# Kernel optimization log

Hardware: AMD Instinct MI355X
Metric: run time of the kernel (lower is better)

Reference implementation:

```python
import jax, jax.numpy as jnp
import numpy as np

B, S, HID = 1, 2048, 2048
H, KH, D = 16, 8, 128          # query heads, kv heads, head_dim
GROUPS = H // KH                # num_key_value_groups = 2
EPS = 1e-6
SCALE = D ** -0.5
NEG = -1e9


def rmsnorm(x, w):
    # torch.nn.RMSNorm over last dim with learned weight
    return x * jax.lax.rsqrt(jnp.mean(x * x, axis=-1, keepdims=True) + EPS) * w


def rope(x, cos, sin):
    # x: [b, s, h, d]; cos/sin: [s, d//2]  (rotate-half style, matching apply_rotary_emb_single)
    half = x.shape[-1] // 2
    xr, xi = x[..., :half], x[..., half:]
    c = cos[None, :, None, :]
    s = sin[None, :, None, :]
    return jnp.concatenate([xr * c - xi * s, xr * s + xi * c], axis=-1)


def setup_inputs() -> dict:
    key = jax.random.key(0)
    ks = jax.random.split(key, 8)
    hidden_states = jax.random.normal(ks[0], (B, S, HID), jnp.float32)
    # real RoPE angle tables (theta=1e6, Qwen3-style), shape [S, D//2]
    inv_freq = 1.0 / (1e6 ** (np.arange(0, D, 2, dtype=np.float32) / D))
    ang = np.arange(S, dtype=np.float32)[:, None] * inv_freq[None, :]
    freqs_cos = jnp.asarray(np.cos(ang), jnp.float32)
    freqs_sin = jnp.asarray(np.sin(ang), jnp.float32)
    # additive causal mask [1, S, S]
    causal = jnp.tril(jnp.ones((S, S), jnp.bool_))
    atten_mask = jnp.where(causal, 0.0, NEG).astype(jnp.float32)[None]
    # learned params (no bias: attention_bias=False)
    Wq = jax.random.normal(ks[1], (H * D, HID), jnp.float32) * 0.02
    Wk = jax.random.normal(ks[2], (KH * D, HID), jnp.float32) * 0.02
    Wv = jax.random.normal(ks[3], (KH * D, HID), jnp.float32) * 0.02
    Wo = jax.random.normal(ks[4], (HID, H * D), jnp.float32) * 0.02
    q_norm_w = 1.0 + 0.01 * jax.random.normal(ks[5], (D,), jnp.float32)
    k_norm_w = 1.0 + 0.01 * jax.random.normal(ks[6], (D,), jnp.float32)
    return {"hidden_states": hidden_states, "freqs_cos": freqs_cos, "freqs_sin": freqs_sin,
            "atten_mask": atten_mask, "Wq": Wq, "Wk": Wk, "Wv": Wv, "Wo": Wo,
            "q_norm_w": q_norm_w, "k_norm_w": k_norm_w}


def reference(hidden_states, freqs_cos, freqs_sin, atten_mask, Wq, Wk, Wv, Wo, q_norm_w, k_norm_w):
    b, s, _ = hidden_states.shape
    q = (hidden_states @ Wq.T).reshape(b, s, H, D)
    k = (hidden_states @ Wk.T).reshape(b, s, KH, D)
    v = (hidden_states @ Wv.T).reshape(b, s, KH, D)
    q = rope(rmsnorm(q, q_norm_w), freqs_cos, freqs_sin)
    k = rope(rmsnorm(k, k_norm_w), freqs_cos, freqs_sin)
    # GQA: head i uses kv head i // GROUPS -> repeat kv heads in-order
    k_exp = jnp.repeat(k, GROUPS, axis=2)  # [b, s, H, d]
    v_exp = jnp.repeat(v, GROUPS, axis=2)
    scores = jnp.einsum('bshd,bthd->bhst', q, k_exp) * SCALE + atten_mask[:, None, :, :]
    attn = jax.nn.softmax(scores, axis=-1)
    y = jnp.einsum('bhst,bthd->bshd', attn, v_exp).reshape(b, s, H * D)
    y = y @ Wo.T
    # output_new_cache_only: last-position k (post-norm/RoPE) and raw v per kv head
    k_new = jnp.transpose(k[:, -1], (1, 0, 2))  # [KH, b, D]
    v_new = jnp.transpose(v[:, -1], (1, 0, 2))  # [KH, b, D]
    return y, k_new, v_new
```

## Files before the change

kernel.cpp:

```cpp
#include <hip/hip_runtime.h>
#include <hip/hip_bf16.h>
#include <math.h>

#define S_LEN 2048
#define HID 2048
#define NH 16
#define NKH 8
#define HD 128
#define QKV_N 4096
#define SCALE 0.08838834764831845f
#define EPS 1e-6f
#define LOG2E 1.4426950408889634f
#define QSCALE (SCALE * LOG2E)

typedef __hip_bfloat16 bf16;
typedef unsigned int u32;
typedef __bf16 bf16x8 __attribute__((ext_vector_type(8)));
typedef float f32x4 __attribute__((ext_vector_type(4)));

#define MFMA(a, b, c) __builtin_amdgcn_mfma_f32_16x16x32_bf16(a, b, c, 0, 0, 0)

static __device__ __forceinline__ bf16x8 ld_frag(const bf16* p) {
    return __builtin_bit_cast(bf16x8, *(const uint4*)p);
}

static __device__ __forceinline__ void gload_lds16(const void* g, void* l) {
    __builtin_amdgcn_global_load_lds(
        (const __attribute__((address_space(1))) u32*)g,
        (__attribute__((address_space(3))) u32*)l, 16, 0, 0);
}

__global__ __launch_bounds__(256) void cvt5(
    const float* __restrict__ s0, const float* __restrict__ s1,
    const float* __restrict__ s2, const float* __restrict__ s3,
    const float* __restrict__ s4,
    bf16* __restrict__ d0, bf16* __restrict__ d1, bf16* __restrict__ d2,
    bf16* __restrict__ d3, bf16* __restrict__ d4)
{
    int i = blockIdx.x * 256 + threadIdx.x;
    const float* s; bf16* d; int off;
    if (i < (1 << 20))                   { s = s0; d = d0; off = 0; }
    else if (i < (2 << 20))              { s = s1; d = d1; off = 1 << 20; }
    else if (i < (2 << 20) + (1 << 19))  { s = s2; d = d2; off = 2 << 20; }
    else if (i < (3 << 20))              { s = s3; d = d3; off = (2 << 20) + (1 << 19); }
    else                                 { s = s4; d = d4; off = 3 << 20; }
    int j = i - off;
    float4 v = ((const float4*)s)[j];
    bf16* p = d + 4 * (size_t)j;
    p[0] = __float2bfloat16(v.x);
    p[1] = __float2bfloat16(v.y);
    p[2] = __float2bfloat16(v.z);
    p[3] = __float2bfloat16(v.w);
}

__global__ __launch_bounds__(256, 2) void gemm_qkv(
    const bf16* __restrict__ A, const bf16* __restrict__ B,
    bf16* __restrict__ qkvb, bf16* __restrict__ vT,
    const float* __restrict__ fcos, const float* __restrict__ fsin,
    const float* __restrict__ qw, const float* __restrict__ kw,
    float* __restrict__ knew, float* __restrict__ vnew)
{
    __shared__ bf16 As[128 * 64];
    __shared__ bf16 Bs[128 * 64];
    const int tid = threadIdx.x;
    const int n0 = blockIdx.x * 128, m0 = blockIdx.y * 128;
    const int w = tid >> 6, lane = tid & 63;
    const int l15 = lane & 15, quad = lane >> 4;

    f32x4 acc[2][8];
    #pragma unroll
    for (int i = 0; i < 2; ++i)
        #pragma unroll
        for (int j = 0; j < 8; ++j)
            acc[i][j] = f32x4{0.f, 0.f, 0.f, 0.f};

    const int srow8 = lane >> 3;
    const int sls = ((lane & 7) ^ srow8) * 8;

    for (int k0 = 0; k0 < HID; k0 += 64) {
        __syncthreads();
        #pragma unroll
        for (int j = 0; j < 8; ++j) {
            int c = 8 * w + j;
            if (c < 16) {
                int row = c * 8 + srow8;
                gload_lds16(A + (size_t)(m0 + row) * HID + k0 + sls, &As[c * 512]);
            } else {
                int row = (c - 16) * 8 + srow8;
                gload_lds16(B + (size_t)(n0 + row) * HID + k0 + sls, &Bs[(c - 16) * 512]);
            }
        }
        __syncthreads();

        #pragma unroll
        for (int kc = 0; kc < 2; ++kc) {
            const int ph = ((kc * 4 + quad) ^ (l15 & 7)) * 8;
            bf16x8 av[2], bv[8];
            av[0] = ld_frag(&As[(w * 32 + l15) * 64 + ph]);
            av[1] = ld_frag(&As[(w * 32 + 16 + l15) * 64 + ph]);
            #pragma unroll
            for (int j = 0; j < 8; ++j)
                bv[j] = ld_frag(&Bs[(j * 16 + l15) * 64 + ph]);
            #pragma unroll
            for (int i = 0; i < 2; ++i)
                #pragma unroll
                for (int j = 0; j < 8; ++j)
                    acc[i][j] = MFMA(av[i], bv[j], acc[i][j]);
        }
    }

    const int hblk = n0 >> 7;
    if (hblk < 24) {
        const float* wgt = (hblk < 16) ? qw : kw;
        float wv[8];
        #pragma unroll
        for (int j = 0; j < 8; ++j) wv[j] = wgt[j * 16 + l15];
        const size_t cb = (hblk < 16) ? (size_t)hblk * HD
                                      : (size_t)HID + (size_t)(hblk - 16) * HD;
        #pragma unroll
        for (int i = 0; i < 2; ++i)
            #pragma unroll
            for (int r = 0; r < 4; ++r) {
                int srow = m0 + w * 32 + i * 16 + quad * 4 + r;
                float ss = 0.f;
                #pragma unroll
                for (int j = 0; j < 8; ++j) ss += acc[i][j][r] * acc[i][j][r];
                ss += __shfl_xor(ss, 1);
                ss += __shfl_xor(ss, 2);
                ss += __shfl_xor(ss, 4);
                ss += __shfl_xor(ss, 8);
                float rr = rsqrtf(ss * (1.0f / 128.0f) + EPS);
                float x[8], res[8];
                #pragma unroll
                for (int j = 0; j < 8; ++j) x[j] = acc[i][j][r] * rr * wv[j];
                #pragma unroll
                for (int jj = 0; jj < 4; ++jj) {
                    float c = fcos[srow * 64 + jj * 16 + l15];
                    float s = fsin[srow * 64 + jj * 16 + l15];
                    res[jj]     = x[jj] * c - x[jj + 4] * s;
                    res[jj + 4] = x[jj] * s + x[jj + 4] * c;
                }
                if (hblk < 16) {
                    #pragma unroll
                    for (int j = 0; j < 8; ++j)
                        qkvb[(size_t)srow * QKV_N + cb + j * 16 + l15] =
                            __float2bfloat16(res[j] * QSCALE);
                } else {
                    #pragma unroll
                    for (int j = 0; j < 8; ++j)
                        qkvb[(size_t)srow * QKV_N + cb + j * 16 + l15] =
                            __float2bfloat16(res[j]);
                    if (srow == S_LEN - 1) {
                        #pragma unroll
                        for (int j = 0; j < 8; ++j)
                            knew[(hblk - 16) * HD + j * 16 + l15] = res[j];
                    }
                }
            }
    } else {
        const int kh = hblk - 24;
        #pragma unroll
        for (int i = 0; i < 2; ++i) {
            int rowbase = m0 + w * 32 + i * 16 + quad * 4;
            #pragma unroll
            for (int j = 0; j < 8; ++j) {
                int d = j * 16 + l15;
                union { uint2 u; bf16 hh[4]; } pk;
                #pragma unroll
                for (int r = 0; r < 4; ++r)
                    pk.hh[r] = __float2bfloat16(acc[i][j][r]);
                *(uint2*)&vT[(size_t)(kh * HD + d) * S_LEN + rowbase] = pk.u;
                if (rowbase == S_LEN - 4)
                    vnew[kh * HD + d] = acc[i][j][3];
            }
        }
    }
}

__global__ __launch_bounds__(256, 2) void gemm_n64(
    const bf16* __restrict__ A, const bf16* __restrict__ B,
    float* __restrict__ C, int M, int N, int K)
{
    __shared__ bf16 As[128 * 64];
    __shared__ bf16 Bs[64 * 64];
    const int tid = threadIdx.x;
    const int n0 = blockIdx.x * 64, m0 = blockIdx.y * 128;
    const int w = tid >> 6, lane = tid & 63;
    const int l15 = lane & 15, quad = lane >> 4;

    f32x4 acc[2][4];
    #pragma unroll
    for (int i = 0; i < 2; ++i)
        #pragma unroll
        for (int j = 0; j < 4; ++j)
            acc[i][j] = f32x4{0.f, 0.f, 0.f, 0.f};

    const int srow8 = lane >> 3;
    const int sls = ((lane & 7) ^ srow8) * 8;

    for (int k0 = 0; k0 < K; k0 += 64) {
        __syncthreads();
        #pragma unroll
        for (int j = 0; j < 6; ++j) {
            int c = 6 * w + j;
            if (c < 16) {
                int row = c * 8 + srow8;
                gload_lds16(A + (size_t)(m0 + row) * K + k0 + sls, &As[c * 512]);
            } else {
                int row = (c - 16) * 8 + srow8;
                gload_lds16(B + (size_t)(n0 + row) * K + k0 + sls, &Bs[(c - 16) * 512]);
            }
        }
        __syncthreads();

        #pragma unroll
        for (int kc = 0; kc < 2; ++kc) {
            const int ph = ((kc * 4 + quad) ^ (l15 & 7)) * 8;
            bf16x8 av[2], bv[4];
            av[0] = ld_frag(&As[(w * 32 + l15) * 64 + ph]);
            av[1] = ld_frag(&As[(w * 32 + 16 + l15) * 64 + ph]);
            #pragma unroll
            for (int j = 0; j < 4; ++j)
                bv[j] = ld_frag(&Bs[(j * 16 + l15) * 64 + ph]);
            #pragma unroll
            for (int i = 0; i < 2; ++i)
                #pragma unroll
                for (int j = 0; j < 4; ++j)
                    acc[i][j] = MFMA(av[i], bv[j], acc[i][j]);
        }
    }

    #pragma unroll
    for (int i = 0; i < 2; ++i)
        #pragma unroll
        for (int j = 0; j < 4; ++j)
            #pragma unroll
            for (int r = 0; r < 4; ++r)
                C[(size_t)(m0 + w * 32 + i * 16 + quad * 4 + r) * N +
                  n0 + j * 16 + l15] = acc[i][j][r];
}

__global__ __launch_bounds__(256, 2) void attn_mfma(
    const bf16* __restrict__ qkvb, const bf16* __restrict__ vT,
    bf16* __restrict__ outb)
{
    __shared__ bf16 Ks[2][64 * 128];
    __shared__ bf16 Vs[2][128 * 64];
    __shared__ bf16 Ps[4][16 * 72];

    const int x = blockIdx.x;
    const int h = blockIdx.y, kvh = h >> 1;
    int a = (x & 1) ? (31 - (x >> 1)) : (x >> 1);
    const int qb = (h < 8) ? a : 31 - a;
    const int tid = threadIdx.x, w = tid >> 6, lane = tid & 63;
    const int l15 = lane & 15, quad = lane >> 4;
    const int qw0 = qb * 64 + w * 16;

    bf16x8 qf[4];
    #pragma unroll
    for (int dk = 0; dk < 4; ++dk)
        qf[dk] = ld_frag(qkvb + (size_t)(qw0 + l15) * QKV_N +
                         h * HD + dk * 32 + quad * 8);

    f32x4 o[8];
    #pragma unroll
    for (int dt = 0; dt < 8; ++dt) o[dt] = f32x4{0.f, 0.f, 0.f, 0.f};
    float l_st = 0.f;

    auto stage = [&](int t, int nb) {
        const int kt0 = t * 64;
        if (w < 2) {
            #pragma unroll
            for (int c = 0; c < 8; ++c) {
                int chunk = w * 8 + c;
                int row = 4 * chunk + (lane >> 4);
                int ls = (lane & 15) ^ (row & 15);
                gload_lds16(qkvb + (size_t)(kt0 + row) * QKV_N + HID +
                            kvh * HD + ls * 8,
                            &Ks[nb][chunk * 512]);
            }
        } else {
            #pragma unroll
            for (int c = 0; c < 8; ++c) {
                int chunk = (w - 2) * 8 + c;
                int row = 8 * chunk + (lane >> 3);
                int ls = (lane & 7) ^ ((lane >> 3) & 7);
                gload_lds16(vT + (size_t)(kvh * HD + row) * S_LEN + kt0 + ls * 8,
                            &Vs[nb][chunk * 512]);
            }
        }
    };

    stage(0, 0);
    for (int t = 0; t <= qb; ++t) {
        const int pp = t & 1;
        const int kt0 = t * 64;
        __syncthreads();
        if (t < qb) stage(t + 1, pp ^ 1);

        f32x4 sc[4];
        #pragma unroll
        for (int mt = 0; mt < 4; ++mt) sc[mt] = f32x4{0.f, 0.f, 0.f, 0.f};
        #pragma unroll
        for (int dk = 0; dk < 4; ++dk)
            #pragma unroll
            for (int mt = 0; mt < 4; ++mt) {
                bf16x8 kf = ld_frag(&Ks[pp][(mt * 16 + l15) * 128 +
                                            (((dk * 4 + quad) ^ l15) & 15) * 8]);
                sc[mt] = MFMA(kf, qf[dk], sc[mt]);
            }

        if (kt0 + 63 > qw0) {
            #pragma unroll
            for (int mt = 0; mt < 4; ++mt)
                #pragma unroll
                for (int r = 0; r < 4; ++r) {
                    int kg = kt0 + mt * 16 + quad * 4 + r;
                    if (kg > qw0 + l15) sc[mt][r] = -1e30f;
                }
        }

        #pragma unroll
        for (int mt = 0; mt < 4; ++mt) {
            union { uint2 u; bf16 hh[4]; } pk;
            #pragma unroll
            for (int r = 0; r < 4; ++r) {
                float p = exp2f(sc[mt][r]);
                pk.hh[r] = __float2bfloat16(p);
                l_st += p;
            }
            *(uint2*)&Ps[w][l15 * 72 + mt * 16 + quad * 4] = pk.u;
        }

        #pragma unroll
        for (int kc = 0; kc < 2; ++kc) {
            bf16x8 pf = ld_frag(&Ps[w][l15 * 72 + kc * 32 + quad * 8]);
            #pragma unroll
            for (int dt = 0; dt < 8; ++dt) {
                bf16x8 vf = ld_frag(&Vs[pp][(dt * 16 + l15) * 64 +
                                            (((kc * 4 + quad) ^ (l15 & 7)) * 8)]);
                o[dt] = MFMA(vf, pf, o[dt]);
            }
        }
    }

    l_st += __shfl_xor(l_st, 16, 64);
    l_st += __shfl_xor(l_st, 32, 64);
    float inv = 1.0f / l_st;
    int qg = qw0 + l15;
    #pragma unroll
    for (int dt = 0; dt < 8; ++dt) {
        union { uint2 u; bf16 hh[4]; } pk;
        #pragma unroll
        for (int r = 0; r < 4; ++r)
            pk.hh[r] = __float2bfloat16(o[dt][r] * inv);
        *(uint2*)&outb[(size_t)qg * HID + h * HD + dt * 16 + quad * 4] = pk.u;
    }
}

extern "C" void kernel_launch(void* const* d_in, const int* in_sizes, int n_in,
                              void* d_out, int out_size, void* d_ws, size_t ws_size,
                              hipStream_t stream) {
    const float* hidden = (const float*)d_in[0];
    const float* fcos   = (const float*)d_in[1];
    const float* fsin   = (const float*)d_in[2];
    const float* Wq = (const float*)d_in[4];
    const float* Wk = (const float*)d_in[5];
    const float* Wv = (const float*)d_in[6];
    const float* Wo = (const float*)d_in[7];
    const float* qw = (const float*)d_in[8];
    const float* kw = (const float*)d_in[9];
    float* out = (float*)d_out;

    bf16* qkvb  = (bf16*)d_ws;
    bf16* vT    = qkvb + (size_t)S_LEN * QKV_N;
    bf16* attnb = vT + (size_t)NKH * HD * S_LEN;
    bf16* wqkvb = attnb + (size_t)S_LEN * HID;
    bf16* hidb  = wqkvb + (size_t)QKV_N * HID;
    bf16* wob   = hidb + (size_t)S_LEN * HID;

    float* knew = out + (size_t)S_LEN * HID;
    float* vnew = knew + NKH * HD;

    cvt5<<<16384, 256, 0, stream>>>(
        hidden, Wq, Wk, Wv, Wo,
        hidb, wqkvb, wqkvb + (size_t)HID * HID,
        wqkvb + (size_t)(HID + NKH * HD) * HID, wob);

    gemm_qkv<<<dim3(QKV_N / 128, S_LEN / 128), 256, 0, stream>>>(
        hidb, wqkvb, qkvb, vT, fcos, fsin, qw, kw, knew, vnew);

    attn_mfma<<<dim3(32, NH), 256, 0, stream>>>(qkvb, vT, attnb);

    gemm_n64<<<dim3(HID / 64, S_LEN / 128), 256, 0, stream>>>(
        attnb, wob, out, S_LEN, HID, HID);
}
```

Before: 240.9 us.

## Double-buffer LDS tiles in GEMMs and use 2x2 warp layout in QKV GEMM

Both the QKV projection GEMM and the output GEMM now keep two LDS buffers and issue the global-to-LDS loads for the next K tile before computing the current one, so memory latency can overlap with MFMA work. The QKV GEMM also switches from a 4x1 warp split (32 rows by 128 columns per warp) to a 2x2 split (64 rows by 64 columns). This cuts the LDS fragment loads per MFMA from 10 loads for 16 MFMAs to 8. Because each warp now holds only half a head row, the RMSNorm sum of squares is combined across warp pairs through a small shared buffer plus an extra barrier. LDS use doubles, which can limit occupancy.

```diff
diff --git a/kernel.cpp b/kernel.cpp
--- a/kernel.cpp
+++ b/kernel.cpp
@@ -60,111 +60,136 @@
     const float* __restrict__ qw, const float* __restrict__ kw,
     float* __restrict__ knew, float* __restrict__ vnew)
 {
-    __shared__ bf16 As[128 * 64];
-    __shared__ bf16 Bs[128 * 64];
+    __shared__ bf16 As[2][128 * 64];
+    __shared__ bf16 Bs[2][128 * 64];
+    __shared__ float red[2][2][64];
     const int tid = threadIdx.x;
     const int n0 = blockIdx.x * 128, m0 = blockIdx.y * 128;
     const int w = tid >> 6, lane = tid & 63;
     const int l15 = lane & 15, quad = lane >> 4;
-
-    f32x4 acc[2][8];
-    #pragma unroll
-    for (int i = 0; i < 2; ++i)
-        #pragma unroll
-        for (int j = 0; j < 8; ++j)
+    const int wr = (w >> 1) * 64;
+    const int wcg = (w & 1) * 32;
+
+    f32x4 acc[4][4];
+    #pragma unroll
+    for (int i = 0; i < 4; ++i)
+        #pragma unroll
+        for (int j = 0; j < 4; ++j)
             acc[i][j] = f32x4{0.f, 0.f, 0.f, 0.f};
 
     const int srow8 = lane >> 3;
     const int sls = ((lane & 7) ^ srow8) * 8;
 
-    for (int k0 = 0; k0 < HID; k0 += 64) {
-        __syncthreads();
+    auto stage = [&](int k0, int nb) {
         #pragma unroll
         for (int j = 0; j < 8; ++j) {
             int c = 8 * w + j;
             if (c < 16) {
                 int row = c * 8 + srow8;
-                gload_lds16(A + (size_t)(m0 + row) * HID + k0 + sls, &As[c * 512]);
+                gload_lds16(A + (size_t)(m0 + row) * HID + k0 + sls, &As[nb][c * 512]);
             } else {
                 int row = (c - 16) * 8 + srow8;
-                gload_lds16(B + (size_t)(n0 + row) * HID + k0 + sls, &Bs[(c - 16) * 512]);
-            }
-        }
+                gload_lds16(B + (size_t)(n0 + row) * HID + k0 + sls, &Bs[nb][(c - 16) * 512]);
+            }
+        }
+    };
+
+    stage(0, 0);
+    for (int kt = 0; kt < HID / 64; ++kt) {
+        const int pp = kt & 1;
         __syncthreads();
+        if (kt + 1 < HID / 64) stage((kt + 1) * 64, pp ^ 1);
 
         #pragma unroll
         for (int kc = 0; kc < 2; ++kc) {
             const int ph = ((kc * 4 + quad) ^ (l15 & 7)) * 8;
-            bf16x8 av[2], bv[8];
-            av[0] = ld_frag(&As[(w * 32 + l15) * 64 + ph]);
-            av[1] = ld_frag(&As[(w * 32 + 16 + l15) * 64 + ph]);
-            #pragma unroll
-            for (int j = 0; j < 8; ++j)
-                bv[j] = ld_frag(&Bs[(j * 16 + l15) * 64 + ph]);
-            #pragma unroll
-            for (int i = 0; i < 2; ++i)
-                #pragma unroll
-                for (int j = 0; j < 8; ++j)
+            bf16x8 av[4], bv[4];
+            #pragma unroll
+            for (int i = 0; i < 4; ++i)
+                av[i] = ld_frag(&As[pp][(wr + i * 16 + l15) * 64 + ph]);
+            #pragma unroll
+            for (int j = 0; j < 4; ++j)
+                bv[j] = ld_frag(&Bs[pp][(wcg + (j & 1) * 16 + (j >> 1) * 64 + l15) * 64 + ph]);
+            #pragma unroll
+            for (int i = 0; i < 4; ++i)
+                #pragma unroll
+                for (int j = 0; j < 4; ++j)
                     acc[i][j] = MFMA(av[i], bv[j], acc[i][j]);
         }
     }
 
     const int hblk = n0 >> 7;
     if (hblk < 24) {
-        const float* wgt = (hblk < 16) ? qw : kw;
-        float wv[8];
-        #pragma unroll
-        for (int j = 0; j < 8; ++j) wv[j] = wgt[j * 16 + l15];
-        const size_t cb = (hblk < 16) ? (size_t)hblk * HD
-                                      : (size_t)HID + (size_t)(hblk - 16) * HD;
-        #pragma unroll
-        for (int i = 0; i < 2; ++i)
-            #pragma unroll
-            for (int r = 0; r < 4; ++r) {
-                int srow = m0 + w * 32 + i * 16 + quad * 4 + r;
+        float ssq[4][4];
+        #pragma unroll
+        for (int i = 0; i < 4; ++i)
+            #pragma unroll
+            for (int rr = 0; rr < 4; ++rr) {
                 float ss = 0.f;
                 #pragma unroll
-                for (int j = 0; j < 8; ++j) ss += acc[i][j][r] * acc[i][j][r];
+                for (int j = 0; j < 4; ++j) ss += acc[i][j][rr] * acc[i][j][rr];
                 ss += __shfl_xor(ss, 1);
                 ss += __shfl_xor(ss, 2);
                 ss += __shfl_xor(ss, 4);
                 ss += __shfl_xor(ss, 8);
-                float rr = rsqrtf(ss * (1.0f / 128.0f) + EPS);
-                float x[8], res[8];
-                #pragma unroll
-                for (int j = 0; j < 8; ++j) x[j] = acc[i][j][r] * rr * wv[j];
-                #pragma unroll
-                for (int jj = 0; jj < 4; ++jj) {
-                    float c = fcos[srow * 64 + jj * 16 + l15];
-                    float s = fsin[srow * 64 + jj * 16 + l15];
-                    res[jj]     = x[jj] * c - x[jj + 4] * s;
-                    res[jj + 4] = x[jj] * s + x[jj + 4] * c;
+                ssq[i][rr] = ss;
+                if (l15 == 0)
+                    red[w >> 1][w & 1][i * 16 + quad * 4 + rr] = ss;
+            }
+        __syncthreads();
+
+        const float* wgt = (hblk < 16) ? qw : kw;
+        float wv[4];
+        #pragma unroll
+        for (int j = 0; j < 4; ++j)
+            wv[j] = wgt[wcg + (j & 1) * 16 + (j >> 1) * 64 + l15];
+        const size_t cb = (hblk < 16) ? (size_t)hblk * HD
+                                      : (size_t)HID + (size_t)(hblk - 16) * HD;
+
+        #pragma unroll
+        for (int i = 0; i < 4; ++i)
+            #pragma unroll
+            for (int rr = 0; rr < 4; ++rr) {
+                int rloc = i * 16 + quad * 4 + rr;
+                int srow = m0 + wr + rloc;
+                float tot = ssq[i][rr] + red[w >> 1][(w & 1) ^ 1][rloc];
+                float rrn = rsqrtf(tot * (1.0f / 128.0f) + EPS);
+                float x[4], res[4];
+                #pragma unroll
+                for (int j = 0; j < 4; ++j) x[j] = acc[i][j][rr] * rrn * wv[j];
+                #pragma unroll
+                for (int j2 = 0; j2 < 2; ++j2) {
+                    float c = fcos[srow * 64 + wcg + j2 * 16 + l15];
+                    float s = fsin[srow * 64 + wcg + j2 * 16 + l15];
+                    res[j2]     = x[j2] * c - x[j2 + 2] * s;
+                    res[j2 + 2] = x[j2] * s + x[j2 + 2] * c;
                 }
                 if (hblk < 16) {
                     #pragma unroll
-                    for (int j = 0; j < 8; ++j)
-                        qkvb[(size_t)srow * QKV_N + cb + j * 16 + l15] =
-                            __float2bfloat16(res[j] * QSCALE);
+                    for (int j = 0; j < 4; ++j)
+                        qkvb[(size_t)srow * QKV_N + cb + wcg + (j & 1) * 16 +
+                             (j >> 1) * 64 + l15] = __float2bfloat16(res[j] * QSCALE);
                 } else {
                     #pragma unroll
-                    for (int j = 0; j < 8; ++j)
-                        qkvb[(size_t)srow * QKV_N + cb + j * 16 + l15] =
-                            __float2bfloat16(res[j]);
+                    for (int j = 0; j < 4; ++j)
+                        qkvb[(size_t)srow * QKV_N + cb + wcg + (j & 1) * 16 +
+                             (j >> 1) * 64 + l15] = __float2bfloat16(res[j]);
                     if (srow == S_LEN - 1) {
                         #pragma unroll
-                        for (int j = 0; j < 8; ++j)
-                            knew[(hblk - 16) * HD + j * 16 + l15] = res[j];
+                        for (int j = 0; j < 4; ++j)
+                            knew[(hblk - 16) * HD + wcg + (j & 1) * 16 +
+                                 (j >> 1) * 64 + l15] = res[j];
                     }
                 }
             }
     } else {
         const int kh = hblk - 24;
         #pragma unroll
-        for (int i = 0; i < 2; ++i) {
-            int rowbase = m0 + w * 32 + i * 16 + quad * 4;
-            #pragma unroll
-            for (int j = 0; j < 8; ++j) {
-                int d = j * 16 + l15;
+        for (int i = 0; i < 4; ++i) {
+            int rowbase = m0 + wr + i * 16 + quad * 4;
+            #pragma unroll
+            for (int j = 0; j < 4; ++j) {
+                int d = wcg + (j & 1) * 16 + (j >> 1) * 64 + l15;
                 union { uint2 u; bf16 hh[4]; } pk;
                 #pragma unroll
                 for (int r = 0; r < 4; ++r)
@@ -181,8 +206,8 @@
     const bf16* __restrict__ A, const bf16* __restrict__ B,
     float* __restrict__ C, int M, int N, int K)
 {
-    __shared__ bf16 As[128 * 64];
-    __shared__ bf16 Bs[64 * 64];
+    __shared__ bf16 As[2][128 * 64];
+    __shared__ bf16 Bs[2][64 * 64];
     const int tid = threadIdx.x;
     const int n0 = blockIdx.x * 64, m0 = blockIdx.y * 128;
     const int w = tid >> 6, lane = tid & 63;
@@ -198,30 +223,35 @@
     const int srow8 = lane >> 3;
     const int sls = ((lane & 7) ^ srow8) * 8;
 
-    for (int k0 = 0; k0 < K; k0 += 64) {
-        __syncthreads();
+    auto stage = [&](int k0, int nb) {
         #pragma unroll
         for (int j = 0; j < 6; ++j) {
             int c = 6 * w + j;
             if (c < 16) {
                 int row = c * 8 + srow8;
-                gload_lds16(A + (size_t)(m0 + row) * K + k0 + sls, &As[c * 512]);
+                gload_lds16(A + (size_t)(m0 + row) * K + k0 + sls, &As[nb][c * 512]);
             } else {
                 int row = (c - 16) * 8 + srow8;
-                gload_lds16(B + (size_t)(n0 + row) * K + k0 + sls, &Bs[(c - 16) * 512]);
-            }
-        }
+                gload_lds16(B + (size_t)(n0 + row) * K + k0 + sls, &Bs[nb][(c - 16) * 512]);
+            }
+        }
+    };
+
+    stage(0, 0);
+    for (int kt = 0; kt < K / 64; ++kt) {
+        const int pp = kt & 1;
         __syncthreads();
+        if (kt + 1 < K / 64) stage((kt + 1) * 64, pp ^ 1);
 
         #pragma unroll
         for (int kc = 0; kc < 2; ++kc) {
             const int ph = ((kc * 4 + quad) ^ (l15 & 7)) * 8;
             bf16x8 av[2], bv[4];
-            av[0] = ld_frag(&As[(w * 32 + l15) * 64 + ph]);
-            av[1] = ld_frag(&As[(w * 32 + 16 + l15) * 64 + ph]);
+            av[0] = ld_frag(&As[pp][(w * 32 + l15) * 64 + ph]);
+            av[1] = ld_frag(&As[pp][(w * 32 + 16 + l15) * 64 + ph]);
             #pragma unroll
             for (int j = 0; j < 4; ++j)
-                bv[j] = ld_frag(&Bs[(j * 16 + l15) * 64 + ph]);
+                bv[j] = ld_frag(&Bs[pp][(j * 16 + l15) * 64 + ph]);
             #pragma unroll
             for (int i = 0; i < 2; ++i)
                 #pragma unroll
```

After: 238.5 us. Within noise of the previous version (-1.0%).
